# Kernel optimization log

Hardware: AMD Instinct MI355X
Metric: run time of the kernel (lower is better)

The kernel has to match this reference:

```python
import jax, jax.numpy as jnp
import numpy as np

D_MODEL = 2048
NUM_HEADS = 16
HEAD_DIM = D_MODEL // NUM_HEADS
SCALE = HEAD_DIM ** -0.5
ALPHA = 1.0


def setup_inputs() -> dict:
    key = jax.random.key(0)
    ks = jax.random.split(key, 9)
    B, T = 2, 2048
    s = 0.02
    w = lambda k: jax.random.normal(k, (D_MODEL, D_MODEL), jnp.float32) * s
    b = lambda k: jax.random.normal(k, (D_MODEL,), jnp.float32) * s
    return {
        'x': jax.random.normal(ks[0], (B, T, D_MODEL), jnp.float32),
        'q_w': w(ks[1]), 'q_b': b(ks[2]),
        'k_w': w(ks[3]), 'k_b': b(ks[4]),
        'v_w': w(ks[5]), 'v_b': b(ks[6]),
        'o_w': w(ks[7]), 'o_b': b(ks[8]),
    }


def reference(x, q_w, q_b, k_w, k_b, v_w, v_b, o_w, o_b):
    B, T, D = x.shape
    H, HD = NUM_HEADS, HEAD_DIM

    def proj_split(w, bias):
        y = x @ w.T + bias  # torch Linear: x @ W^T + b
        # B T (H D) -> (B H) T D
        return y.reshape(B, T, H, HD).transpose(0, 2, 1, 3).reshape(B * H, T, HD)

    Q = proj_split(q_w, q_b)
    K = proj_split(k_w, k_b)
    V = proj_split(v_w, v_b)

    # Note: original computes S[h,i,j] = K_i . Q_j (K first, Q second)
    S = jnp.einsum('hid,hjd->hij', K, Q) * SCALE  # (B*H, T, T)

    idx = jnp.arange(T)
    delta = idx[:, None] - idx[None, :]  # delta[i,j] = i - j
    # similarity_power_law decay: -(delta**alpha) for delta>=0, else 0
    decay = jnp.where(delta < 0, 0.0, -(delta.astype(jnp.float32) ** ALPHA))
    # causal mask: positions with j > i (delta < 0) set to -inf, then add decay
    S = jnp.where(delta < 0, -jnp.inf, S) + decay

    C = jax.nn.softmax(S, axis=-1)
    attn = jnp.einsum('hij,hjd->hid', C, V)  # (B*H, T, HD)
    # (B H) T D -> B T (H D)
    attn = attn.reshape(B, H, T, HD).transpose(0, 2, 1, 3).reshape(B, T, D)
    return attn @ o_w.T + o_b
```

## Files before the change

kernel.cpp:

```cpp
#include <hip/hip_runtime.h>
#include <hip/hip_bf16.h>
#include <stdint.h>

#define BT    4096
#define DM    2048
#define TSEQ  2048
#define NHEAD 16
#define HD    128
#define QKV_LD 6144
#define ATT_SCALE 0.088388347648318447f
#define WIN   64

typedef __attribute__((ext_vector_type(8))) short short8;
typedef __attribute__((ext_vector_type(4))) float f32x4;

__device__ __forceinline__ uint16_t f2bf(float f) {
  uint32_t u = __float_as_uint(f);
  return (uint16_t)((u + 0x7FFFu + ((u >> 16) & 1u)) >> 16);
}

__device__ __forceinline__ void gload_lds16(const void* g, void* l) {
  __builtin_amdgcn_global_load_lds((__attribute__((address_space(1))) void*)g,
                                   (__attribute__((address_space(3))) void*)l,
                                   16, 0, 0);
}

__global__ __launch_bounds__(256) void prep(const float* __restrict__ x,
                                            const float* __restrict__ qw,
                                            const float* __restrict__ kw,
                                            const float* __restrict__ vw,
                                            const float* __restrict__ ow,
                                            const float* __restrict__ qb,
                                            const float* __restrict__ kb,
                                            const float* __restrict__ vb,
                                            uint16_t* __restrict__ xb,
                                            uint16_t* __restrict__ wqkv,
                                            uint16_t* __restrict__ wo,
                                            float* __restrict__ bcat) {
  const int NX = BT * DM / 4;
  const int NW = DM * DM / 4;
  const int total = NX + 4 * NW;
  int i0 = blockIdx.x * 256 + threadIdx.x;
  for (int idx = i0; idx < total; idx += gridDim.x * 256) {
    const float* src;
    uint16_t* dst;
    int off;
    if (idx < NX)            { src = x;  dst = xb;                          off = idx; }
    else if (idx < NX + NW)  { src = qw; dst = wqkv;                        off = idx - NX; }
    else if (idx < NX + 2*NW){ src = kw; dst = wqkv + (size_t)DM * DM;      off = idx - NX - NW; }
    else if (idx < NX + 3*NW){ src = vw; dst = wqkv + (size_t)2 * DM * DM;  off = idx - NX - 2*NW; }
    else                     { src = ow; dst = wo;                          off = idx - NX - 3*NW; }
    float4 v = ((const float4*)src)[off];
    ushort4 o;
    o.x = f2bf(v.x); o.y = f2bf(v.y); o.z = f2bf(v.z); o.w = f2bf(v.w);
    ((ushort4*)dst)[off] = o;
  }
  if (i0 < 3 * DM) {
    float v = (i0 < DM) ? qb[i0] : (i0 < 2 * DM ? kb[i0 - DM] : vb[i0 - 2 * DM]);
    bcat[i0] = v;
  }
}

__global__ __launch_bounds__(512, 1) void gemm384(const uint16_t* __restrict__ A,
                                                  const uint16_t* __restrict__ B,
                                                  const float* __restrict__ bias,
                                                  uint16_t* __restrict__ Cout) {
  __shared__ uint16_t sm[81920];

  const int tid = threadIdx.x;
  const int l   = tid & 63;
  const int wid = tid >> 6;
  const int wr  = wid >> 2;
  const int wc  = wid & 3;
  const int ln  = l & 15;
  const int g   = l >> 4;

  const int bid = blockIdx.x;
  const int xcd = bid & 7;
  const int idx = bid >> 3;
  const int m0  = ((xcd >> 2) * 8 + (idx >> 2)) << 8;
  const int n0  = ((xcd & 3) * 4 + (idx & 3)) * 384;

  const int s_r = wid * 8 + (l >> 3);
  const int s_c = ((l & 7) ^ ((wid * 4 + (l >> 4)) & 7)) << 3;
  const uint16_t* gA = A + (size_t)(m0 + s_r) * DM + s_c;
  const uint16_t* gB = B + (size_t)(n0 + s_r) * DM + s_c;
  const int sdst = wid * 512;

  const int key  = (ln >> 1) & 7;
  const int pc0  = (g ^ key) << 3;
  const int pc1  = ((4 + g) ^ key) << 3;
  const int aoff = (wr * 128 + ln) * 64;
  const int boff = 16384 + (wc * 96 + ln) * 64;

  f32x4 acc[8][6];
#pragma unroll
  for (int i = 0; i < 8; ++i)
#pragma unroll
    for (int j = 0; j < 6; ++j) acc[i][j] = (f32x4){0.f, 0.f, 0.f, 0.f};

  const int nt = DM >> 6;

#define STA(T, U)                                                                \
  if ((T) < nt) {                                                                \
    const uint16_t* s_ = gA + (size_t)((U) * 128) * DM + (size_t)(T) * 64;       \
    uint16_t* d_ = sm + ((T) & 1) * 40960 + (U) * 8192 + sdst;                   \
    gload_lds16(s_, d_);                                                         \
    gload_lds16(s_ + (size_t)64 * DM, d_ + 4096);                                \
  }
#define STB(T, U)                                                                \
  if ((T) < nt) {                                                                \
    const uint16_t* s_ = gB + (size_t)((U) * 128) * DM + (size_t)(T) * 64;       \
    uint16_t* d_ = sm + ((T) & 1) * 40960 + 16384 + (U) * 8192 + sdst;           \
    gload_lds16(s_, d_);                                                         \
    gload_lds16(s_ + (size_t)64 * DM, d_ + 4096);                                \
  }
#define FENCE() asm volatile("" ::: "memory")

#define MMH(BUFP, MH, PC)                                                        \
  __builtin_amdgcn_s_setprio(1);                                                 \
  _Pragma("unroll")                                                              \
  for (int mi = 0; mi < 4; ++mi) {                                               \
    short8 af = *(const short8*)((BUFP) + aoff + ((MH) * 64 + mi * 16) * 64 + (PC)); \
    _Pragma("unroll")                                                            \
    for (int nj = 0; nj < 6; ++nj)                                               \
      acc[(MH) * 4 + mi][nj] = __builtin_amdgcn_mfma_f32_16x16x32_bf16(          \
          af, bf[nj], acc[(MH) * 4 + mi][nj], 0, 0, 0);                          \
  }                                                                              \
  __builtin_amdgcn_s_setprio(0);

  STA(0, 0); STA(0, 1);
  STB(0, 0); STB(0, 1); STB(0, 2);
  STB(1, 0); STB(1, 1); STB(1, 2);
  asm volatile("s_waitcnt vmcnt(6)" ::: "memory");
  FENCE(); __builtin_amdgcn_s_barrier(); FENCE();

#pragma unroll 1
  for (int t = 0; t < nt; ++t) {
    const uint16_t* bufp = sm + (size_t)(t & 1) * 40960;
    short8 bf[6];
#pragma unroll
    for (int nj = 0; nj < 6; ++nj)
      bf[nj] = *(const short8*)(bufp + boff + nj * 1024 + pc0);
    STA(t + 1, 0);
    MMH(bufp, 0, pc0);
    STA(t + 1, 1);
    MMH(bufp, 1, pc0);
#pragma unroll
    for (int nj = 0; nj < 6; ++nj)
      bf[nj] = *(const short8*)(bufp + boff + nj * 1024 + pc1);
    MMH(bufp, 0, pc1);
    FENCE(); __builtin_amdgcn_s_barrier(); FENCE();
    STB(t + 2, 0); STB(t + 2, 1); STB(t + 2, 2);
    MMH(bufp, 1, pc1);
    FENCE();
    if (t < nt - 2)       asm volatile("s_waitcnt vmcnt(6)" ::: "memory");
    else if (t == nt - 2) asm volatile("s_waitcnt vmcnt(0)" ::: "memory");
    __builtin_amdgcn_s_barrier(); FENCE();
  }
#undef MMH
#undef STA
#undef STB
#undef FENCE

  const int g4 = g * 4;
#pragma unroll
  for (int a = 0; a < 8; ++a) {
    size_t row = (size_t)(m0 + wr * 128 + (a >> 2) * 64 + (a & 3) * 16 + g4);
#pragma unroll
    for (int nj = 0; nj < 6; ++nj) {
      int col = n0 + wc * 96 + nj * 16 + ln;
      float bv = bias[col];
#pragma unroll
      for (int r = 0; r < 4; ++r)
        Cout[(row + r) * QKV_LD + col] = f2bf(acc[a][nj][r] + bv);
    }
  }
}

template <int MF, bool OUT_BF16>
__global__ __launch_bounds__(512, 1) void gemm_p4(const uint16_t* __restrict__ A,
                                                  const uint16_t* __restrict__ B,
                                                  const float* __restrict__ bias,
                                                  void* __restrict__ Cout,
                                                  int M, int N, int K) {
  constexpr int BM   = MF * 32;
  constexpr int ABUF = BM * 32;
  constexpr int BUFE = ABUF + 8192;
  constexpr int MB   = (MF == 8) ? 2 : 4;
  constexpr int NB   = 8 / MB;
  __shared__ uint16_t sm[4 * BUFE];

  const int tid = threadIdx.x;
  const int l   = tid & 63;
  const int wid = tid >> 6;
  const int wr  = wid >> 2;
  const int wc  = wid & 3;
  const int ln  = l & 15;
  const int g   = l >> 4;

  const int nbx    = N >> 8;
  const int bid    = blockIdx.x;
  const int xcd    = bid & 7;
  const int idx    = bid >> 3;
  const int rect_n = nbx / NB;
  const int rect_m = (M / BM) / MB;
  const int m_t    = (xcd / NB) * rect_m + idx / rect_n;
  const int n_t    = (xcd % NB) * rect_n + idx % rect_n;
  const int m0     = m_t * BM;
  const int n0     = n_t << 8;

  const int srow = l >> 2;
  const int gch  = (l & 3) ^ ((l >> 3) & 3);
  const uint16_t* pa  = A + (size_t)(m0 + wid * 16 + srow) * K + gch * 8;
  const uint16_t* pb0 = B + (size_t)(n0 + wid * 16 + srow) * K + gch * 8;
  const uint16_t* pb1 = B + (size_t)(n0 + 128 + wid * 16 + srow) * K + gch * 8;
  const int ldsA  = wid * 512;
  const int ldsB0 = ABUF + wid * 512;
  const int ldsB1 = ABUF + 4096 + wid * 512;

  const int pc = g ^ ((ln >> 1) & 3);

  f32x4 acc[MF][4];
#pragma unroll
  for (int i = 0; i < MF; ++i)
#pragma unroll
    for (int j = 0; j < 4; ++j) acc[i][j] = (f32x4){0.f, 0.f, 0.f, 0.f};

  const int nt = K >> 5;

#define STAGE(T)                                                        \
  {                                                                     \
    uint16_t* base_ = sm + (size_t)((T) & 3) * BUFE;                    \
    const size_t ko_ = (size_t)(T) * 32;                                \
    gload_lds16(pa + ko_, base_ + ldsA);                                \
    if (MF == 8) gload_lds16(pa + (size_t)128 * K + ko_, base_ + 4096 + ldsA); \
    gload_lds16(pb0 + ko_, base_ + ldsB0);                              \
    gload_lds16(pb1 + ko_, base_ + ldsB1);                              \
  }

#define COMPUTE(T)                                                      \
  {                                                                     \
    const uint16_t* buf_ = sm + (size_t)((T) & 3) * BUFE;               \
    short8 af_[MF], bf_[4];                                             \
    _Pragma("unroll")                                                   \
    for (int fi = 0; fi < MF; ++fi)                                     \
      af_[fi] = *(const short8*)(buf_ + (wr * (MF * 16) + fi * 16 + ln) * 32 + pc * 8); \
    _Pragma("unroll")                                                   \
    for (int fj = 0; fj < 4; ++fj)                                      \
      bf_[fj] = *(const short8*)(buf_ + ABUF + (wc * 64 + fj * 16 + ln) * 32 + pc * 8); \
    __builtin_amdgcn_s_setprio(1);                                      \
    _Pragma("unroll")                                                   \
    for (int fi = 0; fi < MF; ++fi)                                     \
      _Pragma("unroll")                                                 \
      for (int fj = 0; fj < 4; ++fj)                                    \
        acc[fi][fj] = __builtin_amdgcn_mfma_f32_16x16x32_bf16(          \
            af_[fi], bf_[fj], acc[fi][fj], 0, 0, 0);                    \
    __builtin_amdgcn_s_setprio(0);                                      \
  }

#define WAIT_LOOP()                                                     \
  if (MF == 8) asm volatile("s_waitcnt vmcnt(8)" ::: "memory");         \
  else         asm volatile("s_waitcnt vmcnt(6)" ::: "memory");
#define WAIT_PEEL1()                                                    \
  if (MF == 8) asm volatile("s_waitcnt vmcnt(4)" ::: "memory");         \
  else         asm volatile("s_waitcnt vmcnt(3)" ::: "memory");

  STAGE(0); STAGE(1); STAGE(2);
  WAIT_LOOP();
  __builtin_amdgcn_s_barrier();

#pragma unroll 1
  for (int t = 0; t < nt - 3; ++t) {
    STAGE(t + 3);
    COMPUTE(t);
    WAIT_LOOP();
    __builtin_amdgcn_s_barrier();
  }
  COMPUTE(nt - 3);
  WAIT_PEEL1();
  __builtin_amdgcn_s_barrier();
  COMPUTE(nt - 2);
  asm volatile("s_waitcnt vmcnt(0)" ::: "memory");
  __builtin_amdgcn_s_barrier();
  COMPUTE(nt - 1);
#undef STAGE
#undef COMPUTE
#undef WAIT_LOOP
#undef WAIT_PEEL1

  const int g4 = g * 4;
#pragma unroll
  for (int fi = 0; fi < MF; ++fi) {
    size_t row = (size_t)(m0 + wr * (MF * 16) + fi * 16 + g4);
#pragma unroll
    for (int fj = 0; fj < 4; ++fj) {
      int col = n0 + wc * 64 + fj * 16 + ln;
      float bv = bias[col];
#pragma unroll
      for (int r = 0; r < 4; ++r) {
        float v = acc[fi][fj][r] + bv;
        if (OUT_BF16) ((uint16_t*)Cout)[(row + r) * N + col] = f2bf(v);
        else          ((float*)Cout)[(row + r) * N + col] = v;
      }
    }
  }
}

__global__ __launch_bounds__(256) void attn_mfma(const uint16_t* __restrict__ QKV,
                                                 uint16_t* __restrict__ O) {
  __shared__ __align__(16) uint16_t smem[16384 + 17408];
  uint16_t* Qs = smem;
  uint16_t* Vt = smem + 16384;
  uint16_t* Pl = smem;

  const int tid  = threadIdx.x;
  const int lane = tid & 63;
  const int w    = tid >> 6;
  const int g    = lane >> 4;
  const int ln   = lane & 15;

  const int i0 = blockIdx.x * 64;
  const int h  = blockIdx.y;
  const int b  = blockIdx.z;
  const int wb = i0 - 63;
  const size_t hoff  = (size_t)h * HD;
  const size_t bbase = (size_t)b * TSEQ;

#pragma unroll
  for (int it = 0; it < 8; ++it) {
    int s   = it * 256 + tid;
    int row = s >> 4, c = s & 15;
    int j = wb + row;
    if (j >= 0 && j < TSEQ) {
      const uint16_t* gsrc = QKV + (bbase + j) * (size_t)QKV_LD + hoff
                           + (size_t)((c ^ (row & 7)) * 8);
      uint16_t* ldst = Qs + (size_t)(s & ~63) * 8;
      gload_lds16(gsrc, ldst);
    } else {
      uint4 z = {0, 0, 0, 0};
      *(uint4*)(Qs + (size_t)s * 8) = z;
    }
  }

#pragma unroll
  for (int it = 0; it < 4; ++it) {
    int s  = it * 256 + tid;
    int jp = (s & 15) | (it << 4);
    int dc = (s >> 4) & 15;
    int j0 = wb + 2 * jp;
    uint4 va = {0, 0, 0, 0}, vb = {0, 0, 0, 0};
    if (j0 >= 0 && j0 < TSEQ)
      va = *(const uint4*)(QKV + (bbase + j0) * (size_t)QKV_LD + 2 * DM + hoff + dc * 8);
    if (j0 + 1 >= 0 && j0 + 1 < TSEQ)
      vb = *(const uint4*)(QKV + (bbase + j0 + 1) * (size_t)QKV_LD + 2 * DM + hoff + dc * 8);
    const uint16_t* ap = (const uint16_t*)&va;
    const uint16_t* bp = (const uint16_t*)&vb;
#pragma unroll
    for (int t = 0; t < 8; ++t) {
      uint32_t pk = (uint32_t)ap[t] | ((uint32_t)bp[t] << 16);
      *(uint32_t*)(Vt + (size_t)(dc * 8 + t) * 136 + 2 * jp) = pk;
    }
  }

  short8 kreg[4];
  {
    const uint16_t* kp = QKV + (bbase + i0 + w * 16 + ln) * (size_t)QKV_LD
                       + DM + hoff + g * 8;
#pragma unroll
    for (int kc = 0; kc < 4; ++kc) kreg[kc] = *(const short8*)(kp + kc * 32);
  }

  __syncthreads();

  f32x4 acc[8];
#pragma unroll
  for (int nf = 0; nf < 8; ++nf) acc[nf] = (f32x4){0.f, 0.f, 0.f, 0.f};
#pragma unroll
  for (int kc = 0; kc < 4; ++kc) {
#pragma unroll
    for (int nf = 0; nf < 8; ++nf) {
      int row = nf * 16 + ln;
      int chunk = (kc * 4 + g) ^ (row & 7);
      short8 qf = *(const short8*)(Qs + (size_t)row * 128 + chunk * 8);
      acc[nf] = __builtin_amdgcn_mfma_f32_16x16x32_bf16(kreg[kc], qf, acc[nf], 0, 0, 0);
    }
  }

#pragma unroll
  for (int nf = 0; nf < 8; ++nf) {
    int rj = nf * 16 + ln;
    int jg = wb + rj;
#pragma unroll
    for (int r = 0; r < 4; ++r) {
      int il = w * 16 + g * 4 + r;
      int delta = il + 63 - rj;
      float v = acc[nf][r] * ATT_SCALE - (float)delta;
      acc[nf][r] = ((unsigned)delta < 64u && jg >= 0) ? v : -1e30f;
    }
  }

  float inv[4];
#pragma unroll
  for (int r = 0; r < 4; ++r) {
    float mx = acc[0][r];
#pragma unroll
    for (int nf = 1; nf < 8; ++nf) mx = fmaxf(mx, acc[nf][r]);
    mx = fmaxf(mx, __shfl_xor(mx, 1));
    mx = fmaxf(mx, __shfl_xor(mx, 2));
    mx = fmaxf(mx, __shfl_xor(mx, 4));
    mx = fmaxf(mx, __shfl_xor(mx, 8));
    float s = 0.f;
#pragma unroll
    for (int nf = 0; nf < 8; ++nf) {
      float e = __expf(acc[nf][r] - mx);
      acc[nf][r] = e;
      s += e;
    }
    s += __shfl_xor(s, 1);
    s += __shfl_xor(s, 2);
    s += __shfl_xor(s, 4);
    s += __shfl_xor(s, 8);
    inv[r] = 1.0f / s;
  }

  __syncthreads();

#pragma unroll
  for (int nf = 0; nf < 8; ++nf)
#pragma unroll
    for (int r = 0; r < 4; ++r)
      Pl[(size_t)(w * 16 + g * 4 + r) * 136 + nf * 16 + ln] = f2bf(acc[nf][r]);
  asm volatile("s_waitcnt lgkmcnt(0)" ::: "memory");
  __builtin_amdgcn_sched_barrier(0);

  f32x4 o[8];
#pragma unroll
  for (int nf = 0; nf < 8; ++nf) o[nf] = (f32x4){0.f, 0.f, 0.f, 0.f};
#pragma unroll
  for (int kc = 0; kc < 4; ++kc) {
    short8 pa = *(const short8*)(Pl + (size_t)(w * 16 + ln) * 136 + kc * 32 + g * 8);
#pragma unroll
    for (int nf = 0; nf < 8; ++nf) {
      short8 vbf = *(const short8*)(Vt + (size_t)(nf * 16 + ln) * 136 + kc * 32 + g * 8);
      o[nf] = __builtin_amdgcn_mfma_f32_16x16x32_bf16(pa, vbf, o[nf], 0, 0, 0);
    }
  }

  const size_t obase = (bbase + i0 + w * 16) * (size_t)DM + hoff;
#pragma unroll
  for (int nf = 0; nf < 8; ++nf)
#pragma unroll
    for (int r = 0; r < 4; ++r)
      O[obase + (size_t)(g * 4 + r) * DM + nf * 16 + ln] = f2bf(o[nf][r] * inv[r]);
}

extern "C" void kernel_launch(void* const* d_in, const int* in_sizes, int n_in,
                              void* d_out, int out_size, void* d_ws, size_t ws_size,
                              hipStream_t stream) {
  const float* x   = (const float*)d_in[0];
  const float* q_w = (const float*)d_in[1];
  const float* q_b = (const float*)d_in[2];
  const float* k_w = (const float*)d_in[3];
  const float* k_b = (const float*)d_in[4];
  const float* v_w = (const float*)d_in[5];
  const float* v_b = (const float*)d_in[6];
  const float* o_w = (const float*)d_in[7];
  const float* o_b = (const float*)d_in[8];

  char* ws = (char*)d_ws;
  const size_t XB_BYTES   = (size_t)BT * DM * 2;
  const size_t W_BYTES    = (size_t)DM * DM * 2;
  const size_t WQKV_BYTES = 3 * W_BYTES;

  uint16_t* xb   = (uint16_t*)(ws);
  uint16_t* wqkv = (uint16_t*)(ws + XB_BYTES);
  uint16_t* wo   = (uint16_t*)(ws + XB_BYTES + WQKV_BYTES);
  float*    bcat = (float*)   (ws + XB_BYTES + WQKV_BYTES + W_BYTES);
  uint16_t* QKVb = (uint16_t*)(ws + XB_BYTES + WQKV_BYTES + W_BYTES + 24576);

  prep<<<2048, 256, 0, stream>>>(x, q_w, k_w, v_w, o_w, q_b, k_b, v_b,
                                 xb, wqkv, wo, bcat);

  gemm384<<<256, 512, 0, stream>>>(xb, wqkv, bcat, QKVb);

  dim3 ga(TSEQ / 64, NHEAD, 2);
  attn_mfma<<<ga, 256, 0, stream>>>(QKVb, xb);

  gemm_p4<4, false><<<(BT / 128) * (DM / 256), 512, 0, stream>>>(
      xb, wo, o_b, d_out, BT, DM, DM);
}
```

Baseline: 173.3 us.

## Replace output projection GEMM with 256x128-tile double-buffered split-phase kernel

The generic 4-stage gemm_p4 output-projection kernel (128x256 tiles, K-step 32) is replaced by a dedicated gemmO kernel. It uses 256x128 tiles with K-step 64, two LDS buffers, and staggered A/B loads interleaved with MFMA halves, mirroring the structure of the QKV gemm384 kernel. The grid stays at 256 blocks with an XCD-aware tile mapping. The aim is fewer barriers per unit of K work and better overlap of global-to-LDS loads with MFMA. The trade-off is a shallower pipeline (two stages instead of four), which could expose memory latency.

```diff
diff --git a/kernel.cpp b/kernel.cpp
--- a/kernel.cpp
+++ b/kernel.cpp
@@ -161,7 +161,6 @@
 #undef MMH
 #undef STA
 #undef STB
-#undef FENCE
 
   const int g4 = g * 4;
 #pragma unroll
@@ -178,18 +177,11 @@
   }
 }
 
-template <int MF, bool OUT_BF16>
-__global__ __launch_bounds__(512, 1) void gemm_p4(const uint16_t* __restrict__ A,
-                                                  const uint16_t* __restrict__ B,
-                                                  const float* __restrict__ bias,
-                                                  void* __restrict__ Cout,
-                                                  int M, int N, int K) {
-  constexpr int BM   = MF * 32;
-  constexpr int ABUF = BM * 32;
-  constexpr int BUFE = ABUF + 8192;
-  constexpr int MB   = (MF == 8) ? 2 : 4;
-  constexpr int NB   = 8 / MB;
-  __shared__ uint16_t sm[4 * BUFE];
+__global__ __launch_bounds__(512, 1) void gemmO(const uint16_t* __restrict__ A,
+                                                const uint16_t* __restrict__ B,
+                                                const float* __restrict__ bias,
+                                                float* __restrict__ Cout) {
+  __shared__ uint16_t sm[49152];
 
   const int tid = threadIdx.x;
   const int l   = tid & 63;
@@ -199,110 +191,105 @@
   const int ln  = l & 15;
   const int g   = l >> 4;
 
-  const int nbx    = N >> 8;
-  const int bid    = blockIdx.x;
-  const int xcd    = bid & 7;
-  const int idx    = bid >> 3;
-  const int rect_n = nbx / NB;
-  const int rect_m = (M / BM) / MB;
-  const int m_t    = (xcd / NB) * rect_m + idx / rect_n;
-  const int n_t    = (xcd % NB) * rect_n + idx % rect_n;
-  const int m0     = m_t * BM;
-  const int n0     = n_t << 8;
-
-  const int srow = l >> 2;
-  const int gch  = (l & 3) ^ ((l >> 3) & 3);
-  const uint16_t* pa  = A + (size_t)(m0 + wid * 16 + srow) * K + gch * 8;
-  const uint16_t* pb0 = B + (size_t)(n0 + wid * 16 + srow) * K + gch * 8;
-  const uint16_t* pb1 = B + (size_t)(n0 + 128 + wid * 16 + srow) * K + gch * 8;
-  const int ldsA  = wid * 512;
-  const int ldsB0 = ABUF + wid * 512;
-  const int ldsB1 = ABUF + 4096 + wid * 512;
-
-  const int pc = g ^ ((ln >> 1) & 3);
-
-  f32x4 acc[MF][4];
-#pragma unroll
-  for (int i = 0; i < MF; ++i)
-#pragma unroll
-    for (int j = 0; j < 4; ++j) acc[i][j] = (f32x4){0.f, 0.f, 0.f, 0.f};
-
-  const int nt = K >> 5;
-
-#define STAGE(T)                                                        \
-  {                                                                     \
-    uint16_t* base_ = sm + (size_t)((T) & 3) * BUFE;                    \
-    const size_t ko_ = (size_t)(T) * 32;                                \
-    gload_lds16(pa + ko_, base_ + ldsA);                                \
-    if (MF == 8) gload_lds16(pa + (size_t)128 * K + ko_, base_ + 4096 + ldsA); \
-    gload_lds16(pb0 + ko_, base_ + ldsB0);                              \
-    gload_lds16(pb1 + ko_, base_ + ldsB1);                              \
-  }
-
-#define COMPUTE(T)                                                      \
-  {                                                                     \
-    const uint16_t* buf_ = sm + (size_t)((T) & 3) * BUFE;               \
-    short8 af_[MF], bf_[4];                                             \
-    _Pragma("unroll")                                                   \
-    for (int fi = 0; fi < MF; ++fi)                                     \
-      af_[fi] = *(const short8*)(buf_ + (wr * (MF * 16) + fi * 16 + ln) * 32 + pc * 8); \
-    _Pragma("unroll")                                                   \
-    for (int fj = 0; fj < 4; ++fj)                                      \
-      bf_[fj] = *(const short8*)(buf_ + ABUF + (wc * 64 + fj * 16 + ln) * 32 + pc * 8); \
-    __builtin_amdgcn_s_setprio(1);                                      \
-    _Pragma("unroll")                                                   \
-    for (int fi = 0; fi < MF; ++fi)                                     \
-      _Pragma("unroll")                                                 \
-      for (int fj = 0; fj < 4; ++fj)                                    \
-        acc[fi][fj] = __builtin_amdgcn_mfma_f32_16x16x32_bf16(          \
-            af_[fi], bf_[fj], acc[fi][fj], 0, 0, 0);                    \
-    __builtin_amdgcn_s_setprio(0);                                      \
-  }
-
-#define WAIT_LOOP()                                                     \
-  if (MF == 8) asm volatile("s_waitcnt vmcnt(8)" ::: "memory");         \
-  else         asm volatile("s_waitcnt vmcnt(6)" ::: "memory");
-#define WAIT_PEEL1()                                                    \
-  if (MF == 8) asm volatile("s_waitcnt vmcnt(4)" ::: "memory");         \
-  else         asm volatile("s_waitcnt vmcnt(3)" ::: "memory");
-
-  STAGE(0); STAGE(1); STAGE(2);
-  WAIT_LOOP();
-  __builtin_amdgcn_s_barrier();
+  const int bid = blockIdx.x;
+  const int xcd = bid & 7;
+  const int idx = bid >> 3;
+  const int m0  = ((xcd >> 2) * 8 + (idx >> 2)) << 8;
+  const int n0  = ((xcd & 3) * 4 + (idx & 3)) << 7;
+
+  const int s_r = wid * 8 + (l >> 3);
+  const int s_c = ((l & 7) ^ ((wid * 4 + (l >> 4)) & 7)) << 3;
+  const uint16_t* gA = A + (size_t)(m0 + s_r) * DM + s_c;
+  const uint16_t* gB = B + (size_t)(n0 + s_r) * DM + s_c;
+  const int sdst = wid * 512;
+
+  const int key  = (ln >> 1) & 7;
+  const int pc0  = (g ^ key) << 3;
+  const int pc1  = ((4 + g) ^ key) << 3;
+  const int aoff = (wr * 128 + ln) * 64;
+  const int boff = 16384 + (wc * 32 + ln) * 64;
+
+  f32x4 acc[8][2];
+#pragma unroll
+  for (int i = 0; i < 8; ++i)
+#pragma unroll
+    for (int j = 0; j < 2; ++j) acc[i][j] = (f32x4){0.f, 0.f, 0.f, 0.f};
+
+  const int nt = DM >> 6;
+
+#define STA(T, U)                                                                \
+  if ((T) < nt) {                                                                \
+    const uint16_t* s_ = gA + (size_t)((U) * 128) * DM + (size_t)(T) * 64;       \
+    uint16_t* d_ = sm + ((T) & 1) * 24576 + (U) * 8192 + sdst;                   \
+    gload_lds16(s_, d_);                                                         \
+    gload_lds16(s_ + (size_t)64 * DM, d_ + 4096);                                \
+  }
+#define STB(T)                                                                   \
+  if ((T) < nt) {                                                                \
+    const uint16_t* s_ = gB + (size_t)(T) * 64;                                  \
+    uint16_t* d_ = sm + ((T) & 1) * 24576 + 16384 + sdst;                        \
+    gload_lds16(s_, d_);                                                         \
+    gload_lds16(s_ + (size_t)64 * DM, d_ + 4096);                                \
+  }
+#define FENCE() asm volatile("" ::: "memory")
+
+#define MMH(BUFP, MH, PC)                                                        \
+  __builtin_amdgcn_s_setprio(1);                                                 \
+  _Pragma("unroll")                                                              \
+  for (int mi = 0; mi < 4; ++mi) {                                               \
+    short8 af = *(const short8*)((BUFP) + aoff + ((MH) * 64 + mi * 16) * 64 + (PC)); \
+    _Pragma("unroll")                                                            \
+    for (int nj = 0; nj < 2; ++nj)                                               \
+      acc[(MH) * 4 + mi][nj] = __builtin_amdgcn_mfma_f32_16x16x32_bf16(          \
+          af, bf[nj], acc[(MH) * 4 + mi][nj], 0, 0, 0);                          \
+  }                                                                              \
+  __builtin_amdgcn_s_setprio(0);
+
+  STA(0, 0); STA(0, 1);
+  STB(0);
+  STB(1);
+  asm volatile("s_waitcnt vmcnt(2)" ::: "memory");
+  FENCE(); __builtin_amdgcn_s_barrier(); FENCE();
 
 #pragma unroll 1
-  for (int t = 0; t < nt - 3; ++t) {
-    STAGE(t + 3);
-    COMPUTE(t);
-    WAIT_LOOP();
-    __builtin_amdgcn_s_barrier();
-  }
-  COMPUTE(nt - 3);
-  WAIT_PEEL1();
-  __builtin_amdgcn_s_barrier();
-  COMPUTE(nt - 2);
-  asm volatile("s_waitcnt vmcnt(0)" ::: "memory");
-  __builtin_amdgcn_s_barrier();
-  COMPUTE(nt - 1);
-#undef STAGE
-#undef COMPUTE
-#undef WAIT_LOOP
-#undef WAIT_PEEL1
+  for (int t = 0; t < nt; ++t) {
+    const uint16_t* bufp = sm + (size_t)(t & 1) * 24576;
+    short8 bf[2];
+#pragma unroll
+    for (int nj = 0; nj < 2; ++nj)
+      bf[nj] = *(const short8*)(bufp + boff + nj * 1024 + pc0);
+    STA(t + 1, 0);
+    MMH(bufp, 0, pc0);
+    STA(t + 1, 1);
+    MMH(bufp, 1, pc0);
+#pragma unroll
+    for (int nj = 0; nj < 2; ++nj)
+      bf[nj] = *(const short8*)(bufp + boff + nj * 1024 + pc1);
+    MMH(bufp, 0, pc1);
+    FENCE(); __builtin_amdgcn_s_barrier(); FENCE();
+    STB(t + 2);
+    MMH(bufp, 1, pc1);
+    FENCE();
+    if (t < nt - 2)       asm volatile("s_waitcnt vmcnt(2)" ::: "memory");
+    else if (t == nt - 2) asm volatile("s_waitcnt vmcnt(0)" ::: "memory");
+    __builtin_amdgcn_s_barrier(); FENCE();
+  }
+#undef MMH
+#undef STA
+#undef STB
+#undef FENCE
 
   const int g4 = g * 4;
 #pragma unroll
-  for (int fi = 0; fi < MF; ++fi) {
-    size_t row = (size_t)(m0 + wr * (MF * 16) + fi * 16 + g4);
-#pragma unroll
-    for (int fj = 0; fj < 4; ++fj) {
-      int col = n0 + wc * 64 + fj * 16 + ln;
+  for (int a = 0; a < 8; ++a) {
+    size_t row = (size_t)(m0 + wr * 128 + (a >> 2) * 64 + (a & 3) * 16 + g4);
+#pragma unroll
+    for (int nj = 0; nj < 2; ++nj) {
+      int col = n0 + wc * 32 + nj * 16 + ln;
       float bv = bias[col];
 #pragma unroll
-      for (int r = 0; r < 4; ++r) {
-        float v = acc[fi][fj][r] + bv;
-        if (OUT_BF16) ((uint16_t*)Cout)[(row + r) * N + col] = f2bf(v);
-        else          ((float*)Cout)[(row + r) * N + col] = v;
-      }
+      for (int r = 0; r < 4; ++r)
+        Cout[(row + r) * DM + col] = acc[a][nj][r] + bv;
     }
   }
 }
@@ -487,6 +474,5 @@
   dim3 ga(TSEQ / 64, NHEAD, 2);
   attn_mfma<<<ga, 256, 0, stream>>>(QKVb, xb);
 
-  gemm_p4<4, false><<<(BT / 128) * (DM / 256), 512, 0, stream>>>(
-      xb, wo, o_b, d_out, BT, DM, DM);
-}
+  gemmO<<<256, 512, 0, stream>>>(xb, wo, o_b, (float*)d_out);
+}
```

Result: no change. 172.3 us (median of 2 runs) (-0.6%).
